# Kernel tuning notes

Hardware: AMD Instinct MI355X
Metric: run time of the kernel (lower is better)

Reference implementation:

```python
import jax, jax.numpy as jnp
import numpy as np

B, LT, LE, D, H, M, BS = 4, 2048, 1024, 1024, 16, 4096, 128
HD = D // H            # head dim 64
NB = LT // BS          # 16 blocks
SINK_ITERS = 5
NEG = -1e9
SCALE = 1.0 / np.sqrt(HD).astype(np.float32)


def setup_inputs() -> dict:
    key = jax.random.key(0)
    ks = jax.random.split(key, 16)
    p = lambda k, shp: jax.random.normal(k, shp, jnp.float32) * 0.02
    return {
        "targets": jax.random.normal(ks[0], (B, LT, D), jnp.float32),
        "encoded": jax.random.normal(ks[1], (B, LE, D), jnp.float32),
        "ln1_s": jnp.ones((D,), jnp.float32), "ln1_b": jnp.zeros((D,), jnp.float32),
        "ln2_s": jnp.ones((D,), jnp.float32), "ln2_b": jnp.zeros((D,), jnp.float32),
        "ln3_s": jnp.ones((D,), jnp.float32), "ln3_b": jnp.zeros((D,), jnp.float32),
        "wq1": p(ks[2], (D, H, HD)), "wk1": p(ks[3], (D, H, HD)),
        "wv1": p(ks[4], (D, H, HD)), "wo1": p(ks[5], (H, HD, D)),
        "wsort": p(ks[6], (H, HD, NB)),
        "wq2": p(ks[7], (D, H, HD)), "wk2": p(ks[8], (D, H, HD)),
        "wv2": p(ks[9], (D, H, HD)), "wo2": p(ks[10], (H, HD, D)),
        "w1": p(ks[11], (D, M)), "b1": jnp.zeros((M,), jnp.float32),
        "w2": p(ks[12], (M, D)), "b2": jnp.zeros((D,), jnp.float32),
    }


def layer_norm(x, s, b, eps=1e-6):
    mu = jnp.mean(x, -1, keepdims=True)
    var = jnp.mean(jnp.square(x - mu), -1, keepdims=True)
    return (x - mu) * jax.lax.rsqrt(var + eps) * s + b


def causal_sinkhorn(logits):
    # logits: [B,H,NB,NB]. Causal block mask + iterative log-space row/col
    # normalization -> soft (doubly-stochastic-ish) block permutation matrix.
    mask = jnp.tril(jnp.ones((NB, NB), bool))
    la = jnp.where(mask, logits, NEG)
    for _ in range(SINK_ITERS):
        la = la - jax.nn.logsumexp(la, axis=-1, keepdims=True)
        la = jnp.where(mask, la, NEG)
        la = la - jax.nn.logsumexp(la, axis=-2, keepdims=True)
        la = jnp.where(mask, la, NEG)
    return jnp.exp(la)


def sinkhorn_self_attention(x, wq, wk, wv, wsort, wo):
    # x: [B,LT,D] -> blocked q/k/v: [B,NB,BS,H,HD]
    q = jnp.einsum('bld,dhk->blhk', x, wq).reshape(B, NB, BS, H, HD)
    k = jnp.einsum('bld,dhk->blhk', x, wk).reshape(B, NB, BS, H, HD)
    v = jnp.einsum('bld,dhk->blhk', x, wv).reshape(B, NB, BS, H, HD)
    # SortNet: sum-pooled block key representations -> block-to-block logits
    krep = jnp.sum(k, axis=2)                                   # [B,NB,H,HD]
    P = causal_sinkhorn(jnp.einsum('bnhk,hkm->bhnm', krep, wsort))  # [B,H,NB,NB]
    ks = jnp.einsum('bhij,bjshk->bishk', P, k)                  # sorted key blocks
    vs = jnp.einsum('bhij,bjshk->bishk', P, v)
    # each query block attends to (own block [causal]) ++ (sorted block)
    s_loc = jnp.einsum('bnqhk,bnshk->bhnqs', q, k) * SCALE      # [B,H,NB,BS,BS]
    s_srt = jnp.einsum('bnqhk,bnshk->bhnqs', q, ks) * SCALE
    cm = jnp.tril(jnp.ones((BS, BS), bool))
    s_loc = jnp.where(cm, s_loc, NEG)
    w = jax.nn.softmax(jnp.concatenate([s_loc, s_srt], axis=-1), axis=-1)
    o = (jnp.einsum('bhnqs,bnshk->bnqhk', w[..., :BS], v)
         + jnp.einsum('bhnqs,bnshk->bnqhk', w[..., BS:], vs))
    return jnp.einsum('blhk,hkd->bld', o.reshape(B, LT, H, HD), wo)


def cross_attention(x, kv, wq, wk, wv, wo):
    q = jnp.einsum('bld,dhk->blhk', x, wq)
    k = jnp.einsum('bld,dhk->blhk', kv, wk)
    v = jnp.einsum('bld,dhk->blhk', kv, wv)
    w = jax.nn.softmax(jnp.einsum('bqhk,bshk->bhqs', q, k) * SCALE, axis=-1)
    o = jnp.einsum('bhqs,bshk->bqhk', w, v)
    return jnp.einsum('blhk,hkd->bld', o, wo)


def reference(targets, encoded, ln1_s, ln1_b, ln2_s, ln2_b, ln3_s, ln3_b,
              wq1, wk1, wv1, wo1, wsort, wq2, wk2, wv2, wo2, w1, b1, w2, b2):
    x = layer_norm(targets, ln1_s, ln1_b)
    x = sinkhorn_self_attention(x, wq1, wk1, wv1, wsort, wo1) + targets
    y = layer_norm(x, ln2_s, ln2_b)
    y = cross_attention(y, encoded, wq2, wk2, wv2, wo2) + x
    z = layer_norm(y, ln3_s, ln3_b)
    z = jnp.dot(jax.nn.gelu(jnp.dot(z, w1) + b1), w2) + b2
    return y + z
```

## Files before the change

### kernel.cpp

```cpp
#include <hip/hip_runtime.h>

typedef unsigned short u16;
typedef __attribute__((ext_vector_type(8))) short short8;
typedef __attribute__((ext_vector_type(4))) short short4_t;
typedef __attribute__((ext_vector_type(4))) float float4_t;

#define B_ 4
#define LT_ 2048
#define LE_ 1024
#define D_ 1024
#define H_ 16
#define HD_ 64
#define NB_ 16
#define BS_ 128
#define M_ 4096
#define SCALE_ 0.125f

typedef __attribute__((address_space(1))) const void gas_t;
typedef __attribute__((address_space(3))) void las_t;

__device__ __forceinline__ float b2f(u16 u) {
  union { unsigned int i; float f; } v; v.i = ((unsigned int)u) << 16; return v.f;
}
__device__ __forceinline__ u16 f2b(float f) {
  union { float f; unsigned int i; } v; v.f = f;
  unsigned int x = v.i;
  return (u16)((x + 0x7fffu + ((x >> 16) & 1u)) >> 16);
}
__device__ __forceinline__ float gelu_f(float u) {
  float t = 0.7978845608028654f * (u + 0.044715f * u * u * u);
  float th = 1.f - 2.f / (__expf(2.f * t) + 1.f);
  return 0.5f * u * (1.f + th);
}
__device__ __forceinline__ void store_val(u16* p, float x) { *p = f2b(x); }
__device__ __forceinline__ void store_val(float* p, float x) { *p = x; }

__global__ __launch_bounds__(256)
void conv_k(const float* __restrict__ in, u16* __restrict__ out) {
  int i = (blockIdx.x * 256 + threadIdx.x) * 4;
  float4_t v = *(const float4_t*)(in + i);
  short4_t o;
  o[0] = (short)f2b(v[0]); o[1] = (short)f2b(v[1]);
  o[2] = (short)f2b(v[2]); o[3] = (short)f2b(v[3]);
  *(short4_t*)(out + i) = o;
}

__global__ __launch_bounds__(256)
void transpose_k(const float* __restrict__ in, u16* __restrict__ out, int R, int rstride) {
  __shared__ u16 tile[32][33];
  int bx = blockIdx.x * 32, by = blockIdx.y * 32;
  int tx = threadIdx.x & 31, ty = threadIdx.x >> 5;
  #pragma unroll
  for (int y = ty; y < 32; y += 8)
    tile[y][tx] = f2b(in[(size_t)(by + y) * rstride + bx + tx]);
  __syncthreads();
  #pragma unroll
  for (int y = ty; y < 32; y += 8)
    out[(size_t)(bx + y) * R + by + tx] = tile[tx][y];
}

#define NJOBS 10
struct TJobs {
  const float* src[NJOBS];
  u16* dst[NJOBS];
  int outR[NJOBS];
  int inS[NJOBS];
  int ntx[NJOBS];
  int ntiles[NJOBS];
};

__global__ __launch_bounds__(256)
void prep_k(TJobs J) {
  int t = blockIdx.x, j = 0;
  while (t >= J.ntiles[j]) { t -= J.ntiles[j]; ++j; }
  const float* in = J.src[j];
  u16* out = J.dst[j];
  const int R = J.outR[j], rstride = J.inS[j];
  const int bx = (t % J.ntx[j]) * 32, by = (t / J.ntx[j]) * 32;
  __shared__ u16 tile[32][33];
  int tx = threadIdx.x & 31, ty = threadIdx.x >> 5;
  #pragma unroll
  for (int y = ty; y < 32; y += 8)
    tile[y][tx] = f2b(in[(size_t)(by + y) * rstride + bx + tx]);
  __syncthreads();
  #pragma unroll
  for (int y = ty; y < 32; y += 8)
    out[(size_t)(bx + y) * R + by + tx] = tile[tx][y];
}

__global__ __launch_bounds__(256)
void ln_k(const float* __restrict__ x, const float* __restrict__ sw,
          const float* __restrict__ bw, u16* __restrict__ out) {
  int row = blockIdx.x, tid = threadIdx.x;
  const float* xr = x + (size_t)row * 1024 + tid * 4;
  float4_t raw = *(const float4_t*)xr;
  float v0 = raw[0], v1 = raw[1], v2 = raw[2], v3 = raw[3];
  float sum = v0 + v1 + v2 + v3;
  #pragma unroll
  for (int off = 32; off > 0; off >>= 1) sum += __shfl_down(sum, off, 64);
  __shared__ float sA[4], sB[4];
  int w = tid >> 6;
  if ((tid & 63) == 0) sA[w] = sum;
  __syncthreads();
  float mu = (sA[0] + sA[1] + sA[2] + sA[3]) * (1.f / 1024.f);
  float d0 = v0 - mu, d1 = v1 - mu, d2 = v2 - mu, d3 = v3 - mu;
  float s2 = d0 * d0 + d1 * d1 + d2 * d2 + d3 * d3;
  #pragma unroll
  for (int off = 32; off > 0; off >>= 1) s2 += __shfl_down(s2, off, 64);
  if ((tid & 63) == 0) sB[w] = s2;
  __syncthreads();
  float inv = rsqrtf((sB[0] + sB[1] + sB[2] + sB[3]) * (1.f / 1024.f) + 1e-6f);
  float4_t sv = *(const float4_t*)(sw + tid * 4);
  float4_t bv = *(const float4_t*)(bw + tid * 4);
  short4_t ov;
  ov[0] = (short)f2b(d0 * inv * sv[0] + bv[0]);
  ov[1] = (short)f2b(d1 * inv * sv[1] + bv[1]);
  ov[2] = (short)f2b(d2 * inv * sv[2] + bv[2]);
  ov[3] = (short)f2b(d3 * inv * sv[3] + bv[3]);
  *(short4_t*)(out + (size_t)row * 1024 + tid * 4) = ov;
}

template<int EPI, typename TC>
__global__ __launch_bounds__(256)
void gemm_k(const u16* __restrict__ A, const u16* __restrict__ Bt,
            const float* __restrict__ bias, const float* __restrict__ res,
            TC* __restrict__ C, int M, int N, int K) {
  __shared__ __align__(16) u16 lA[128 * 32];
  __shared__ __align__(16) u16 lB[128 * 32];
  const int gx = gridDim.x;
  int lin = blockIdx.y * gx + blockIdx.x;
  const int nwg = gx * gridDim.y;
  if (!(nwg & 7)) {
    const int chunk = nwg >> 3;
    lin = (lin & 7) * chunk + (lin >> 3);
  }
  const int bn = (lin % gx) * 128;
  const int bm = (lin / gx) * 128;
  const int tid = threadIdx.x;
  const int lane = tid & 63;
  const int wave = tid >> 6;
  const int wy = wave >> 1, wx = wave & 1;
  const int quad = lane >> 4, l16 = lane & 15;

  float4_t acc[4][4];
  float4_t zz = {0.f, 0.f, 0.f, 0.f};
  #pragma unroll
  for (int i = 0; i < 4; ++i)
    #pragma unroll
    for (int j = 0; j < 4; ++j) acc[i][j] = zz;

  const int r0 = tid >> 2, kc0 = (tid & 3) * 8;
  const u16* gA0 = A + (size_t)(bm + r0) * K + kc0;
  const u16* gA1 = A + (size_t)(bm + 64 + r0) * K + kc0;
  const u16* gB0 = Bt + (size_t)(bn + r0) * K + kc0;
  const u16* gB1 = Bt + (size_t)(bn + 64 + r0) * K + kc0;
  u16* lA0 = &lA[tid * 8];
  u16* lA1 = &lA[(tid + 256) * 8];
  u16* lB0 = &lB[tid * 8];
  u16* lB1 = &lB[(tid + 256) * 8];

  for (int k0 = 0; k0 < K; k0 += 32) {
    __syncthreads();
    __builtin_amdgcn_global_load_lds((gas_t*)(gA0 + k0), (las_t*)lA0, 16, 0, 0);
    __builtin_amdgcn_global_load_lds((gas_t*)(gA1 + k0), (las_t*)lA1, 16, 0, 0);
    __builtin_amdgcn_global_load_lds((gas_t*)(gB0 + k0), (las_t*)lB0, 16, 0, 0);
    __builtin_amdgcn_global_load_lds((gas_t*)(gB1 + k0), (las_t*)lB1, 16, 0, 0);
    __syncthreads();
    short8 af[4], bfr[4];
    #pragma unroll
    for (int i = 0; i < 4; ++i)
      af[i] = *(const short8*)&lA[(wy * 64 + i * 16 + l16) * 32 + quad * 8];
    #pragma unroll
    for (int j = 0; j < 4; ++j)
      bfr[j] = *(const short8*)&lB[(wx * 64 + j * 16 + l16) * 32 + quad * 8];
    #pragma unroll
    for (int i = 0; i < 4; ++i)
      #pragma unroll
      for (int j = 0; j < 4; ++j)
        acc[i][j] = __builtin_amdgcn_mfma_f32_16x16x32_bf16(af[i], bfr[j], acc[i][j], 0, 0, 0);
  }

  #pragma unroll
  for (int i = 0; i < 4; ++i) {
    int row = bm + wy * 64 + i * 16 + quad * 4;
    #pragma unroll
    for (int j = 0; j < 4; ++j) {
      int col = bn + wx * 64 + j * 16 + l16;
      #pragma unroll
      for (int v = 0; v < 4; ++v) {
        float x = acc[i][j][v];
        size_t idx = (size_t)(row + v) * N + col;
        if (EPI == 1) {
          x += res[idx];
        } else if (EPI == 2) {
          x = gelu_f(x + bias[col]);
        } else if (EPI == 3) {
          x += bias[col] + res[idx];
        }
        store_val(&C[idx], x);
      }
    }
  }
}

__global__ __launch_bounds__(256)
void krep_k(const u16* __restrict__ K1, float* __restrict__ krep) {
  int idx = blockIdx.x * 256 + threadIdx.x;
  int col = idx & 1023;
  int bn = idx >> 10;
  const u16* p = K1 + (size_t)bn * 128 * 1024 + col;
  float s = 0.f;
  for (int i = 0; i < 128; ++i) s += b2f(p[(size_t)i * 1024]);
  krep[idx] = s;
}

__global__ __launch_bounds__(256)
void sinkhorn_k(const float* __restrict__ krep, const float* __restrict__ wsort,
                float* __restrict__ P) {
  int bh = blockIdx.x;
  int b = bh >> 4, h = bh & 15;
  int t = threadIdx.x;
  int i = t >> 4, j = t & 15;
  __shared__ float la[16][17];
  __shared__ float red[16];
  float acc = 0.f;
  const float* kr = krep + ((size_t)b * 16 + i) * 1024 + h * 64;
  const float* ws = wsort + (size_t)h * 64 * 16 + j;
  for (int k = 0; k < 64; ++k) acc += kr[k] * ws[k * 16];
  la[i][j] = (j <= i) ? acc : -1e9f;
  __syncthreads();
  for (int it = 0; it < 5; ++it) {
    if (t < 16) {
      float m = -1e30f;
      for (int jj = 0; jj < 16; ++jj) m = fmaxf(m, la[t][jj]);
      float s = 0.f;
      for (int jj = 0; jj < 16; ++jj) s += __expf(la[t][jj] - m);
      red[t] = m + __logf(s);
    }
    __syncthreads();
    la[i][j] = (j <= i) ? la[i][j] - red[i] : -1e9f;
    __syncthreads();
    if (t < 16) {
      float m = -1e30f;
      for (int ii = 0; ii < 16; ++ii) m = fmaxf(m, la[ii][t]);
      float s = 0.f;
      for (int ii = 0; ii < 16; ++ii) s += __expf(la[ii][t] - m);
      red[t] = m + __logf(s);
    }
    __syncthreads();
    la[i][j] = (j <= i) ? la[i][j] - red[j] : -1e9f;
    __syncthreads();
  }
  P[((size_t)bh * 16 + i) * 16 + j] = __expf(la[i][j]);
}

__global__ __launch_bounds__(256)
void sortmix_k(const float* __restrict__ P, const u16* __restrict__ K1,
               const u16* __restrict__ V1, u16* __restrict__ KS,
               u16* __restrict__ VS) {
  int t = blockIdx.x * 256 + threadIdx.x;
  int col = (t & 127) * 8;
  int rest = t >> 7;
  int b = rest >> 11, is = rest & 2047, i = is >> 7, s = is & 127;
  int h = col >> 6;
  const float* Pr = P + (((size_t)(b * 16 + h)) * 16 + i) * 16;
  size_t base = ((size_t)(b * 2048 + s)) * 1024 + col;
  float ka[8] = {0, 0, 0, 0, 0, 0, 0, 0}, va[8] = {0, 0, 0, 0, 0, 0, 0, 0};
  for (int j = 0; j <= i; ++j) {
    float p = Pr[j];
    short8 kk = *(const short8*)&K1[base + (size_t)j * 131072];
    short8 vv = *(const short8*)&V1[base + (size_t)j * 131072];
    #pragma unroll
    for (int e = 0; e < 8; ++e) {
      ka[e] += p * b2f((u16)kk[e]);
      va[e] += p * b2f((u16)vv[e]);
    }
  }
  size_t ob = ((size_t)(b * 2048 + i * 128 + s)) * 1024 + col;
  short8 ok, ov;
  #pragma unroll
  for (int e = 0; e < 8; ++e) { ok[e] = (short)f2b(ka[e]); ov[e] = (short)f2b(va[e]); }
  *(short8*)&KS[ob] = ok;
  *(short8*)&VS[ob] = ov;
}

#define KLS 72
#define VTS 136
#define PLS 136

template<int CROSS>
__global__ __launch_bounds__(256)
void attn_mfma_k(const u16* __restrict__ Q, const u16* __restrict__ Ka,
                 const u16* __restrict__ Va, const u16* __restrict__ Kb2,
                 const u16* __restrict__ Vb2, u16* __restrict__ O) {
  __shared__ __align__(16) u16 kls[128 * KLS];
  __shared__ __align__(16) u16 vtls[64 * VTS];
  __shared__ __align__(16) u16 pls[128 * PLS];
  const int blk = blockIdx.x;
  const int n = blk & 15, h = (blk >> 4) & 15, b = blk >> 8;
  const int tid = threadIdx.x, lane = tid & 63, wv = tid >> 6;
  const int quad = lane >> 4, l16 = lane & 15;
  const int m0 = wv * 32;
  const size_t qrowbase = (size_t)b * 2048 + n * 128;

  short8 qa[2][2];
  #pragma unroll
  for (int qi = 0; qi < 2; ++qi)
    #pragma unroll
    for (int ks = 0; ks < 2; ++ks)
      qa[qi][ks] = *(const short8*)&Q[(qrowbase + m0 + qi * 16 + l16) * 1024 +
                                      h * 64 + ks * 32 + quad * 8];

  float4_t acc_o[2][4];
  float mrow[2], lrow[2];
  #pragma unroll
  for (int mi = 0; mi < 2; ++mi) {
    #pragma unroll
    for (int dn = 0; dn < 4; ++dn) acc_o[mi][dn] = {0.f, 0.f, 0.f, 0.f};
    mrow[mi] = -1e30f; lrow[mi] = 0.f;
  }

  const int NT = CROSS ? 8 : 2;
  for (int t = 0; t < NT; ++t) {
    const u16 *Kg, *Vg;
    bool causal = false;
    if (CROSS) {
      size_t kb = ((size_t)b * 1024 + t * 128) * 1024 + h * 64;
      Kg = Ka + kb; Vg = Va + kb;
    } else if (t == 0) {
      size_t kb = qrowbase * 1024 + h * 64;
      Kg = Ka + kb; Vg = Va + kb; causal = true;
    } else {
      size_t kb = qrowbase * 1024 + h * 64;
      Kg = Kb2 + kb; Vg = Vb2 + kb;
    }
    __syncthreads();
    #pragma unroll
    for (int i = 0; i < 4; ++i) {
      int c = tid + i * 256;
      int row = c >> 3, dd = (c & 7) * 8;
      short8 kv = *(const short8*)&Kg[(size_t)row * 1024 + dd];
      *(short8*)&kls[row * KLS + dd] = kv;
      short8 vv = *(const short8*)&Vg[(size_t)row * 1024 + dd];
      #pragma unroll
      for (int e = 0; e < 8; ++e) vtls[(dd + e) * VTS + row] = (u16)vv[e];
    }
    __syncthreads();

    float4_t s[2][8];
    #pragma unroll
    for (int qi = 0; qi < 2; ++qi)
      #pragma unroll
      for (int nj = 0; nj < 8; ++nj) s[qi][nj] = {0.f, 0.f, 0.f, 0.f};
    #pragma unroll
    for (int nj = 0; nj < 8; ++nj) {
      short8 k0 = *(const short8*)&kls[(nj * 16 + l16) * KLS + quad * 8];
      short8 k1 = *(const short8*)&kls[(nj * 16 + l16) * KLS + 32 + quad * 8];
      #pragma unroll
      for (int qi = 0; qi < 2; ++qi) {
        s[qi][nj] = __builtin_amdgcn_mfma_f32_16x16x32_bf16(k0, qa[qi][0], s[qi][nj], 0, 0, 0);
        s[qi][nj] = __builtin_amdgcn_mfma_f32_16x16x32_bf16(k1, qa[qi][1], s[qi][nj], 0, 0, 0);
      }
    }

    float crv[2];
    #pragma unroll
    for (int qi = 0; qi < 2; ++qi) {
      const int qrow = m0 + qi * 16 + l16;
      float mx = -1e30f;
      #pragma unroll
      for (int nj = 0; nj < 8; ++nj)
        #pragma unroll
        for (int v = 0; v < 4; ++v) {
          float x = s[qi][nj][v] * SCALE_;
          if (causal && (nj * 16 + quad * 4 + v > qrow)) x = -1e30f;
          s[qi][nj][v] = x;
          mx = fmaxf(mx, x);
        }
      mx = fmaxf(mx, __shfl_xor(mx, 16, 64));
      mx = fmaxf(mx, __shfl_xor(mx, 32, 64));
      float mn = fmaxf(mrow[qi], mx);
      crv[qi] = __expf(mrow[qi] - mn);
      mrow[qi] = mn;
      float rs = 0.f;
      #pragma unroll
      for (int nj = 0; nj < 8; ++nj)
        #pragma unroll
        for (int v = 0; v < 4; ++v) {
          float p = __expf(s[qi][nj][v] - mn);
          s[qi][nj][v] = p;
          rs += p;
        }
      rs += __shfl_xor(rs, 16, 64);
      rs += __shfl_xor(rs, 32, 64);
      lrow[qi] = lrow[qi] * crv[qi] + rs;
      #pragma unroll
      for (int nj = 0; nj < 8; ++nj) {
        unsigned p01 = (unsigned)f2b(s[qi][nj][0]) | ((unsigned)f2b(s[qi][nj][1]) << 16);
        unsigned p23 = (unsigned)f2b(s[qi][nj][2]) | ((unsigned)f2b(s[qi][nj][3]) << 16);
        *(unsigned*)&pls[qrow * PLS + nj * 16 + quad * 4] = p01;
        *(unsigned*)&pls[qrow * PLS + nj * 16 + quad * 4 + 2] = p23;
      }
    }
    #pragma unroll
    for (int mi = 0; mi < 2; ++mi)
      #pragma unroll
      for (int v = 0; v < 4; ++v) {
        float c = __shfl(crv[mi], quad * 20 + v, 64);
        #pragma unroll
        for (int dn = 0; dn < 4; ++dn) acc_o[mi][dn][v] *= c;
      }

    #pragma unroll
    for (int ks = 0; ks < 4; ++ks) {
      short8 a0 = *(const short8*)&pls[(m0 + l16) * PLS + ks * 32 + quad * 8];
      short8 a1 = *(const short8*)&pls[(m0 + 16 + l16) * PLS + ks * 32 + quad * 8];
      #pragma unroll
      for (int dn = 0; dn < 4; ++dn) {
        short8 bv = *(const short8*)&vtls[(dn * 16 + l16) * VTS + ks * 32 + quad * 8];
        acc_o[0][dn] = __builtin_amdgcn_mfma_f32_16x16x32_bf16(a0, bv, acc_o[0][dn], 0, 0, 0);
        acc_o[1][dn] = __builtin_amdgcn_mfma_f32_16x16x32_bf16(a1, bv, acc_o[1][dn], 0, 0, 0);
      }
    }
  }
  #pragma unroll
  for (int mi = 0; mi < 2; ++mi) {
    float invl = 1.f / lrow[mi];
    #pragma unroll
    for (int v = 0; v < 4; ++v) {
      float inv = __shfl(invl, quad * 20 + v, 64);
      int rowl = m0 + mi * 16 + quad * 4 + v;
      #pragma unroll
      for (int dn = 0; dn < 4; ++dn)
        O[(qrowbase + rowl) * 1024 + h * 64 + dn * 16 + l16] =
            f2b(acc_o[mi][dn][v] * inv);
    }
  }
}

extern "C" void kernel_launch(void* const* d_in, const int* in_sizes, int n_in,
                              void* d_out, int out_size, void* d_ws, size_t ws_size,
                              hipStream_t stream) {
  const float* targets = (const float*)d_in[0];
  const float* encoded = (const float*)d_in[1];
  const float* ln1s = (const float*)d_in[2];
  const float* ln1b = (const float*)d_in[3];
  const float* ln2s = (const float*)d_in[4];
  const float* ln2b = (const float*)d_in[5];
  const float* ln3s = (const float*)d_in[6];
  const float* ln3b = (const float*)d_in[7];
  const float* wq1 = (const float*)d_in[8];
  const float* wk1 = (const float*)d_in[9];
  const float* wv1 = (const float*)d_in[10];
  const float* wo1 = (const float*)d_in[11];
  const float* wsort = (const float*)d_in[12];
  const float* wq2 = (const float*)d_in[13];
  const float* wk2 = (const float*)d_in[14];
  const float* wv2 = (const float*)d_in[15];
  const float* wo2 = (const float*)d_in[16];
  const float* w1 = (const float*)d_in[17];
  const float* b1 = (const float*)d_in[18];
  const float* w2 = (const float*)d_in[19];
  const float* b2 = (const float*)d_in[20];
  float* out = (float*)d_out;
  (void)in_sizes; (void)n_in; (void)out_size;

  char* ws = (char*)d_ws;
  size_t off = 0;
  auto alloc = [&](size_t n) -> char* {
    char* p = ws + off;
    off += (n + 255) & ~(size_t)255;
    return p;
  };

  const size_t NTD = (size_t)B_ * LT_ * D_;
  const size_t NEED_BIG = (size_t)(8 * 2 + 8 + 8) * 1024 * 1024
                        + (size_t)LE_ * B_ * D_ * 2
                        + NTD * 2 * 7
                        + (1u << 20);

  if (ws_size >= NEED_BIG) {
    u16* wq1t = (u16*)alloc((size_t)1024 * 1024 * 2);
    u16* wk1t = (u16*)alloc((size_t)1024 * 1024 * 2);
    u16* wv1t = (u16*)alloc((size_t)1024 * 1024 * 2);
    u16* wo1t = (u16*)alloc((size_t)1024 * 1024 * 2);
    u16* wq2t = (u16*)alloc((size_t)1024 * 1024 * 2);
    u16* wk2t = (u16*)alloc((size_t)1024 * 1024 * 2);
    u16* wv2t = (u16*)alloc((size_t)1024 * 1024 * 2);
    u16* wo2t = (u16*)alloc((size_t)1024 * 1024 * 2);
    u16* w1t = (u16*)alloc((size_t)4096 * 1024 * 2);
    u16* w2t = (u16*)alloc((size_t)1024 * 4096 * 2);
    u16* Eb  = (u16*)alloc((size_t)B_ * LE_ * D_ * 2);
    u16* XLN = (u16*)alloc(NTD * 2);
    u16* Qb  = (u16*)alloc(NTD * 2);
    u16* Kb  = (u16*)alloc(NTD * 2);
    u16* Vb  = (u16*)alloc(NTD * 2);
    u16* KSb = (u16*)alloc(NTD * 2);
    u16* VSb = (u16*)alloc(NTD * 2);
    u16* Ob  = (u16*)alloc(NTD * 2);
    float* KREP = (float*)alloc((size_t)B_ * NB_ * 1024 * 4);
    float* Pm = (float*)alloc((size_t)B_ * H_ * NB_ * NB_ * 4);
    u16* HML = Qb;

    TJobs J;
    const float* srcs[NJOBS] = {wq1, wk1, wv1, wo1, wq2, wk2, wv2, wo2, w1, w2};
    u16* dsts[NJOBS] = {wq1t, wk1t, wv1t, wo1t, wq2t, wk2t, wv2t, wo2t, w1t, w2t};
    int total = 0;
    for (int j = 0; j < NJOBS; ++j) {
      J.src[j] = srcs[j]; J.dst[j] = dsts[j];
      if (j < 8)      { J.outR[j] = 1024; J.inS[j] = 1024; J.ntx[j] = 32;  J.ntiles[j] = 1024; }
      else if (j == 8){ J.outR[j] = 1024; J.inS[j] = 4096; J.ntx[j] = 128; J.ntiles[j] = 4096; }
      else            { J.outR[j] = 4096; J.inS[j] = 1024; J.ntx[j] = 32;  J.ntiles[j] = 4096; }
      total += J.ntiles[j];
    }
    prep_k<<<total, 256, 0, stream>>>(J);
    conv_k<<<4096, 256, 0, stream>>>(encoded, Eb);

    ln_k<<<8192, 256, 0, stream>>>(targets, ln1s, ln1b, XLN);
    gemm_k<0, u16><<<dim3(8, 64), 256, 0, stream>>>(XLN, wq1t, nullptr, nullptr, Qb, 8192, 1024, 1024);
    gemm_k<0, u16><<<dim3(8, 64), 256, 0, stream>>>(XLN, wk1t, nullptr, nullptr, Kb, 8192, 1024, 1024);
    gemm_k<0, u16><<<dim3(8, 64), 256, 0, stream>>>(XLN, wv1t, nullptr, nullptr, Vb, 8192, 1024, 1024);
    krep_k<<<256, 256, 0, stream>>>(Kb, KREP);
    sinkhorn_k<<<64, 256, 0, stream>>>(KREP, wsort, Pm);
    sortmix_k<<<4096, 256, 0, stream>>>(Pm, Kb, Vb, KSb, VSb);
    attn_mfma_k<0><<<1024, 256, 0, stream>>>(Qb, Kb, Vb, KSb, VSb, Ob);
    gemm_k<1, float><<<dim3(8, 64), 256, 0, stream>>>(Ob, wo1t, nullptr, targets, out, 8192, 1024, 1024);
    ln_k<<<8192, 256, 0, stream>>>(out, ln2s, ln2b, XLN);
    gemm_k<0, u16><<<dim3(8, 64), 256, 0, stream>>>(XLN, wq2t, nullptr, nullptr, Qb, 8192, 1024, 1024);
    gemm_k<0, u16><<<dim3(8, 32), 256, 0, stream>>>(Eb, wk2t, nullptr, nullptr, Kb, 4096, 1024, 1024);
    gemm_k<0, u16><<<dim3(8, 32), 256, 0, stream>>>(Eb, wv2t, nullptr, nullptr, Vb, 4096, 1024, 1024);
    attn_mfma_k<1><<<1024, 256, 0, stream>>>(Qb, Kb, Vb, nullptr, nullptr, Ob);
    gemm_k<1, float><<<dim3(8, 64), 256, 0, stream>>>(Ob, wo2t, nullptr, out, out, 8192, 1024, 1024);
    ln_k<<<8192, 256, 0, stream>>>(out, ln3s, ln3b, XLN);
    gemm_k<2, u16><<<dim3(32, 64), 256, 0, stream>>>(XLN, w1t, b1, nullptr, HML, 8192, 4096, 1024);
    gemm_k<3, float><<<dim3(8, 64), 256, 0, stream>>>(HML, w2t, b2, out, out, 8192, 1024, 4096);
    return;
  }

  const size_t SLC = (size_t)LT_ * D_;
  u16* wT  = (u16*)alloc((size_t)1024 * 1024 * 2);
  u16* XLN = (u16*)alloc(SLC * 2);
  u16* Qb  = (u16*)alloc(SLC * 2);
  u16* Kb  = (u16*)alloc(SLC * 2);
  u16* Vb  = (u16*)alloc(SLC * 2);
  u16* KSb = (u16*)alloc(SLC * 2);
  u16* VSb = (u16*)alloc(SLC * 2);
  u16* Ob  = (u16*)alloc(SLC * 2);
  u16* Hc  = (u16*)alloc(SLC * 2);
  u16* Eb  = (u16*)alloc((size_t)LE_ * D_ * 2);
  float* KREP = (float*)alloc((size_t)NB_ * 1024 * 4);
  float* Pm = (float*)alloc((size_t)H_ * NB_ * NB_ * 4);

  auto T = [&](const float* src, int rs) {
    transpose_k<<<dim3(32, 32), 256, 0, stream>>>(src, wT, 1024, rs);
  };

  for (int b = 0; b < B_; ++b) {
    const float* tgt_b = targets + (size_t)b * SLC;
    const float* enc_b = encoded + (size_t)b * LE_ * D_;
    float* out_b = out + (size_t)b * SLC;

    ln_k<<<2048, 256, 0, stream>>>(tgt_b, ln1s, ln1b, XLN);
    T(wq1, 1024);
    gemm_k<0, u16><<<dim3(8, 16), 256, 0, stream>>>(XLN, wT, nullptr, nullptr, Qb, 2048, 1024, 1024);
    T(wk1, 1024);
    gemm_k<0, u16><<<dim3(8, 16), 256, 0, stream>>>(XLN, wT, nullptr, nullptr, Kb, 2048, 1024, 1024);
    T(wv1, 1024);
    gemm_k<0, u16><<<dim3(8, 16), 256, 0, stream>>>(XLN, wT, nullptr, nullptr, Vb, 2048, 1024, 1024);
    krep_k<<<64, 256, 0, stream>>>(Kb, KREP);
    sinkhorn_k<<<16, 256, 0, stream>>>(KREP, wsort, Pm);
    sortmix_k<<<1024, 256, 0, stream>>>(Pm, Kb, Vb, KSb, VSb);
    attn_mfma_k<0><<<256, 256, 0, stream>>>(Qb, Kb, Vb, KSb, VSb, Ob);
    T(wo1, 1024);
    gemm_k<1, float><<<dim3(8, 16), 256, 0, stream>>>(Ob, wT, nullptr, tgt_b, out_b, 2048, 1024, 1024);
    ln_k<<<2048, 256, 0, stream>>>(out_b, ln2s, ln2b, XLN);
    conv_k<<<1024, 256, 0, stream>>>(enc_b, Eb);
    T(wq2, 1024);
    gemm_k<0, u16><<<dim3(8, 16), 256, 0, stream>>>(XLN, wT, nullptr, nullptr, Qb, 2048, 1024, 1024);
    T(wk2, 1024);
    gemm_k<0, u16><<<dim3(8, 8), 256, 0, stream>>>(Eb, wT, nullptr, nullptr, Kb, 1024, 1024, 1024);
    T(wv2, 1024);
    gemm_k<0, u16><<<dim3(8, 8), 256, 0, stream>>>(Eb, wT, nullptr, nullptr, Vb, 1024, 1024, 1024);
    attn_mfma_k<1><<<256, 256, 0, stream>>>(Qb, Kb, Vb, nullptr, nullptr, Ob);
    T(wo2, 1024);
    gemm_k<1, float><<<dim3(8, 16), 256, 0, stream>>>(Ob, wT, nullptr, out_b, out_b, 2048, 1024, 1024);
    ln_k<<<2048, 256, 0, stream>>>(out_b, ln3s, ln3b, XLN);
    for (int c = 0; c < 4; ++c) {
      T(w1 + (size_t)c * 1024, 4096);
      gemm_k<2, u16><<<dim3(8, 16), 256, 0, stream>>>(XLN, wT, b1 + c * 1024, nullptr, Hc,
                                                      2048, 1024, 1024);
      T(w2 + (size_t)c * 1024 * 1024, 1024);
      if (c < 3)
        gemm_k<1, float><<<dim3(8, 16), 256, 0, stream>>>(Hc, wT, nullptr, out_b, out_b,
                                                          2048, 1024, 1024);
      else
        gemm_k<3, float><<<dim3(8, 16), 256, 0, stream>>>(Hc, wT, b2, out_b, out_b,
                                                          2048, 1024, 1024);
    }
  }
}
```

Before: 824.5 us.

## Fuse QKV projections into split-output GEMMs and add 256x256 pipelined GEMM kernel

Adds a 256x256-tile, 512-thread GEMM kernel with a 4-stage global_load_lds pipeline and swizzled LDS reads. It is used for a fused Q/K/V projection (N=3072) and the FFN up-projection. The cross-attention K/V projections are fused into one launch using a split-output epilogue that writes each 1024-column slice into a separate buffer. The aim is fewer launches, better operand reuse and more latency hiding, at the cost of relying on the Q/K/V and weight buffers being laid out contiguously at a stride of NTD.

After: 794.3 us. 3.7% less time.

```diff
diff --git a/kernel.cpp b/kernel.cpp
--- a/kernel.cpp
+++ b/kernel.cpp
@@ -120,11 +120,11 @@
   *(short4_t*)(out + (size_t)row * 1024 + tid * 4) = ov;
 }
 
-template<int EPI, typename TC>
+template<int EPI, typename TC, int SPLIT>
 __global__ __launch_bounds__(256)
 void gemm_k(const u16* __restrict__ A, const u16* __restrict__ Bt,
             const float* __restrict__ bias, const float* __restrict__ res,
-            TC* __restrict__ C, int M, int N, int K) {
+            TC* __restrict__ C, int M, int N, int K, size_t cstride) {
   __shared__ __align__(16) u16 lA[128 * 32];
   __shared__ __align__(16) u16 lB[128 * 32];
   const int gx = gridDim.x;
@@ -186,10 +186,13 @@
     #pragma unroll
     for (int j = 0; j < 4; ++j) {
       int col = bn + wx * 64 + j * 16 + l16;
+      TC* Cb = SPLIT ? (C + (size_t)(col >> 10) * cstride) : C;
+      int ccol = SPLIT ? (col & 1023) : col;
+      int cn = SPLIT ? 1024 : N;
       #pragma unroll
       for (int v = 0; v < 4; ++v) {
         float x = acc[i][j][v];
-        size_t idx = (size_t)(row + v) * N + col;
+        size_t idx = (size_t)(row + v) * cn + ccol;
         if (EPI == 1) {
           x += res[idx];
         } else if (EPI == 2) {
@@ -197,7 +200,121 @@
         } else if (EPI == 3) {
           x += bias[col] + res[idx];
         }
-        store_val(&C[idx], x);
+        store_val(&Cb[idx], x);
+      }
+    }
+  }
+}
+
+template<int EPI, typename TC, int SPLIT>
+__global__ __launch_bounds__(512, 2)
+void gemm256_k(const u16* __restrict__ A, const u16* __restrict__ Bt,
+               const float* __restrict__ bias, const float* __restrict__ res,
+               TC* __restrict__ C, int M, int N, int K, size_t cstride) {
+  __shared__ __align__(16) u16 lA[4][256 * 32];
+  __shared__ __align__(16) u16 lB[4][256 * 32];
+  const int gx = gridDim.x;
+  int lin = blockIdx.y * gx + blockIdx.x;
+  const int nwg = gx * gridDim.y;
+  if (!(nwg & 7)) {
+    const int chunk = nwg >> 3;
+    lin = (lin & 7) * chunk + (lin >> 3);
+  }
+  const int bn = (lin % gx) * 256;
+  const int bm = (lin / gx) * 256;
+  const int tid = threadIdx.x;
+  const int lane = tid & 63;
+  const int wave = tid >> 6;
+  const int wy = wave >> 2, wx = wave & 3;
+  const int quad = lane >> 4, l16 = lane & 15;
+  const int slo = ((quad ^ ((l16 >> 1) & 3)) << 4);
+
+  int lrow[2], kcs[2];
+  #pragma unroll
+  for (int u = 0; u < 2; ++u) {
+    int p = (tid + u * 512) * 16;
+    int lg = p ^ (((p >> 7) & 3) << 4);
+    lrow[u] = lg >> 6;
+    kcs[u] = (lg & 63) >> 1;
+  }
+  const u16* gA[2]; const u16* gB[2];
+  #pragma unroll
+  for (int u = 0; u < 2; ++u) {
+    gA[u] = A + (size_t)(bm + lrow[u]) * K + kcs[u];
+    gB[u] = Bt + (size_t)(bn + lrow[u]) * K + kcs[u];
+  }
+  const int NT = K >> 5;
+
+  float4_t acc[8][4];
+  float4_t zz = {0.f, 0.f, 0.f, 0.f};
+  #pragma unroll
+  for (int i = 0; i < 8; ++i)
+    #pragma unroll
+    for (int j = 0; j < 4; ++j) acc[i][j] = zz;
+
+  #define STAGE256(TT, BUF)                                                      \
+    {                                                                            \
+      int kk_ = (TT) * 32;                                                       \
+      __builtin_amdgcn_global_load_lds((gas_t*)(gA[0] + kk_),                    \
+          (las_t*)((char*)&lA[BUF][0] + tid * 16), 16, 0, 0);                    \
+      __builtin_amdgcn_global_load_lds((gas_t*)(gA[1] + kk_),                    \
+          (las_t*)((char*)&lA[BUF][0] + (tid + 512) * 16), 16, 0, 0);            \
+      __builtin_amdgcn_global_load_lds((gas_t*)(gB[0] + kk_),                    \
+          (las_t*)((char*)&lB[BUF][0] + tid * 16), 16, 0, 0);                    \
+      __builtin_amdgcn_global_load_lds((gas_t*)(gB[1] + kk_),                    \
+          (las_t*)((char*)&lB[BUF][0] + (tid + 512) * 16), 16, 0, 0);            \
+    }
+
+  STAGE256(0, 0)
+  STAGE256(1, 1)
+  STAGE256(2, 2)
+
+  for (int t = 0; t < NT; ++t) {
+    asm volatile("s_waitcnt vmcnt(8)" ::: "memory");
+    __builtin_amdgcn_s_barrier();
+    __builtin_amdgcn_sched_barrier(0);
+    int ts = t + 3; if (ts > NT - 1) ts = NT - 1;
+    STAGE256(ts, (t + 3) & 3)
+    const char* bufA = (const char*)&lA[t & 3][0];
+    const char* bufB = (const char*)&lB[t & 3][0];
+    short8 af[8], bf[4];
+    #pragma unroll
+    for (int i = 0; i < 8; ++i)
+      af[i] = *(const short8*)(bufA + (wy * 128 + i * 16 + l16) * 64 + slo);
+    #pragma unroll
+    for (int j = 0; j < 4; ++j)
+      bf[j] = *(const short8*)(bufB + (wx * 64 + j * 16 + l16) * 64 + slo);
+    __builtin_amdgcn_s_setprio(1);
+    #pragma unroll
+    for (int i = 0; i < 8; ++i)
+      #pragma unroll
+      for (int j = 0; j < 4; ++j)
+        acc[i][j] = __builtin_amdgcn_mfma_f32_16x16x32_bf16(af[i], bf[j], acc[i][j], 0, 0, 0);
+    __builtin_amdgcn_s_setprio(0);
+  }
+  #undef STAGE256
+
+  #pragma unroll
+  for (int i = 0; i < 8; ++i) {
+    int row = bm + wy * 128 + i * 16 + quad * 4;
+    #pragma unroll
+    for (int j = 0; j < 4; ++j) {
+      int col = bn + wx * 64 + j * 16 + l16;
+      TC* Cb = SPLIT ? (C + (size_t)(col >> 10) * cstride) : C;
+      int ccol = SPLIT ? (col & 1023) : col;
+      int cn = SPLIT ? 1024 : N;
+      #pragma unroll
+      for (int v = 0; v < 4; ++v) {
+        float x = acc[i][j][v];
+        size_t idx = (size_t)(row + v) * cn + ccol;
+        if (EPI == 1) {
+          x += res[idx];
+        } else if (EPI == 2) {
+          x = gelu_f(x + bias[col]);
+        } else if (EPI == 3) {
+          x += bias[col] + res[idx];
+        }
+        store_val(&Cb[idx], x);
       }
     }
   }
@@ -517,23 +634,21 @@
     conv_k<<<4096, 256, 0, stream>>>(encoded, Eb);
 
     ln_k<<<8192, 256, 0, stream>>>(targets, ln1s, ln1b, XLN);
-    gemm_k<0, u16><<<dim3(8, 64), 256, 0, stream>>>(XLN, wq1t, nullptr, nullptr, Qb, 8192, 1024, 1024);
-    gemm_k<0, u16><<<dim3(8, 64), 256, 0, stream>>>(XLN, wk1t, nullptr, nullptr, Kb, 8192, 1024, 1024);
-    gemm_k<0, u16><<<dim3(8, 64), 256, 0, stream>>>(XLN, wv1t, nullptr, nullptr, Vb, 8192, 1024, 1024);
+    gemm256_k<0, u16, 1><<<dim3(12, 32), 512, 0, stream>>>(XLN, wq1t, nullptr, nullptr,
+                                                           Qb, 8192, 3072, 1024, NTD);
     krep_k<<<256, 256, 0, stream>>>(Kb, KREP);
     sinkhorn_k<<<64, 256, 0, stream>>>(KREP, wsort, Pm);
     sortmix_k<<<4096, 256, 0, stream>>>(Pm, Kb, Vb, KSb, VSb);
     attn_mfma_k<0><<<1024, 256, 0, stream>>>(Qb, Kb, Vb, KSb, VSb, Ob);
-    gemm_k<1, float><<<dim3(8, 64), 256, 0, stream>>>(Ob, wo1t, nullptr, targets, out, 8192, 1024, 1024);
+    gemm_k<1, float, 0><<<dim3(8, 64), 256, 0, stream>>>(Ob, wo1t, nullptr, targets, out, 8192, 1024, 1024, 0);
     ln_k<<<8192, 256, 0, stream>>>(out, ln2s, ln2b, XLN);
-    gemm_k<0, u16><<<dim3(8, 64), 256, 0, stream>>>(XLN, wq2t, nullptr, nullptr, Qb, 8192, 1024, 1024);
-    gemm_k<0, u16><<<dim3(8, 32), 256, 0, stream>>>(Eb, wk2t, nullptr, nullptr, Kb, 4096, 1024, 1024);
-    gemm_k<0, u16><<<dim3(8, 32), 256, 0, stream>>>(Eb, wv2t, nullptr, nullptr, Vb, 4096, 1024, 1024);
+    gemm_k<0, u16, 0><<<dim3(8, 64), 256, 0, stream>>>(XLN, wq2t, nullptr, nullptr, Qb, 8192, 1024, 1024, 0);
+    gemm_k<0, u16, 1><<<dim3(16, 32), 256, 0, stream>>>(Eb, wk2t, nullptr, nullptr, Kb, 4096, 2048, 1024, NTD);
     attn_mfma_k<1><<<1024, 256, 0, stream>>>(Qb, Kb, Vb, nullptr, nullptr, Ob);
-    gemm_k<1, float><<<dim3(8, 64), 256, 0, stream>>>(Ob, wo2t, nullptr, out, out, 8192, 1024, 1024);
+    gemm_k<1, float, 0><<<dim3(8, 64), 256, 0, stream>>>(Ob, wo2t, nullptr, out, out, 8192, 1024, 1024, 0);
     ln_k<<<8192, 256, 0, stream>>>(out, ln3s, ln3b, XLN);
-    gemm_k<2, u16><<<dim3(32, 64), 256, 0, stream>>>(XLN, w1t, b1, nullptr, HML, 8192, 4096, 1024);
-    gemm_k<3, float><<<dim3(8, 64), 256, 0, stream>>>(HML, w2t, b2, out, out, 8192, 1024, 4096);
+    gemm256_k<2, u16, 0><<<dim3(16, 32), 512, 0, stream>>>(XLN, w1t, b1, nullptr, HML, 8192, 4096, 1024, 0);
+    gemm_k<3, float, 0><<<dim3(8, 64), 256, 0, stream>>>(HML, w2t, b2, out, out, 8192, 1024, 4096, 0);
     return;
   }
 
@@ -562,40 +677,40 @@
 
     ln_k<<<2048, 256, 0, stream>>>(tgt_b, ln1s, ln1b, XLN);
     T(wq1, 1024);
-    gemm_k<0, u16><<<dim3(8, 16), 256, 0, stream>>>(XLN, wT, nullptr, nullptr, Qb, 2048, 1024, 1024);
+    gemm_k<0, u16, 0><<<dim3(8, 16), 256, 0, stream>>>(XLN, wT, nullptr, nullptr, Qb, 2048, 1024, 1024, 0);
     T(wk1, 1024);
-    gemm_k<0, u16><<<dim3(8, 16), 256, 0, stream>>>(XLN, wT, nullptr, nullptr, Kb, 2048, 1024, 1024);
+    gemm_k<0, u16, 0><<<dim3(8, 16), 256, 0, stream>>>(XLN, wT, nullptr, nullptr, Kb, 2048, 1024, 1024, 0);
     T(wv1, 1024);
-    gemm_k<0, u16><<<dim3(8, 16), 256, 0, stream>>>(XLN, wT, nullptr, nullptr, Vb, 2048, 1024, 1024);
+    gemm_k<0, u16, 0><<<dim3(8, 16), 256, 0, stream>>>(XLN, wT, nullptr, nullptr, Vb, 2048, 1024, 1024, 0);
     krep_k<<<64, 256, 0, stream>>>(Kb, KREP);
     sinkhorn_k<<<16, 256, 0, stream>>>(KREP, wsort, Pm);
     sortmix_k<<<1024, 256, 0, stream>>>(Pm, Kb, Vb, KSb, VSb);
     attn_mfma_k<0><<<256, 256, 0, stream>>>(Qb, Kb, Vb, KSb, VSb, Ob);
     T(wo1, 1024);
-    gemm_k<1, float><<<dim3(8, 16), 256, 0, stream>>>(Ob, wT, nullptr, tgt_b, out_b, 2048, 1024, 1024);
+    gemm_k<1, float, 0><<<dim3(8, 16), 256, 0, stream>>>(Ob, wT, nullptr, tgt_b, out_b, 2048, 1024, 1024, 0);
     ln_k<<<2048, 256, 0, stream>>>(out_b, ln2s, ln2b, XLN);
     conv_k<<<1024, 256, 0, stream>>>(enc_b, Eb);
     T(wq2, 1024);
-    gemm_k<0, u16><<<dim3(8, 16), 256, 0, stream>>>(XLN, wT, nullptr, nullptr, Qb, 2048, 1024, 1024);
+    gemm_k<0, u16, 0><<<dim3(8, 16), 256, 0, stream>>>(XLN, wT, nullptr, nullptr, Qb, 2048, 1024, 1024, 0);
     T(wk2, 1024);
-    gemm_k<0, u16><<<dim3(8, 8), 256, 0, stream>>>(Eb, wT, nullptr, nullptr, Kb, 1024, 1024, 1024);
+    gemm_k<0, u16, 0><<<dim3(8, 8), 256, 0, stream>>>(Eb, wT, nullptr, nullptr, Kb, 1024, 1024, 1024, 0);
     T(wv2, 1024);
-    gemm_k<0, u16><<<dim3(8, 8), 256, 0, stream>>>(Eb, wT, nullptr, nullptr, Vb, 1024, 1024, 1024);
+    gemm_k<0, u16, 0><<<dim3(8, 8), 256, 0, stream>>>(Eb, wT, nullptr, nullptr, Vb, 1024, 1024, 1024, 0);
     attn_mfma_k<1><<<256, 256, 0, stream>>>(Qb, Kb, Vb, nullptr, nullptr, Ob);
     T(wo2, 1024);
-    gemm_k<1, float><<<dim3(8, 16), 256, 0, stream>>>(Ob, wT, nullptr, out_b, out_b, 2048, 1024, 1024);
+    gemm_k<1, float, 0><<<dim3(8, 16), 256, 0, stream>>>(Ob, wT, nullptr, out_b, out_b, 2048, 1024, 1024, 0);
     ln_k<<<2048, 256, 0, stream>>>(out_b, ln3s, ln3b, XLN);
     for (int c = 0; c < 4; ++c) {
       T(w1 + (size_t)c * 1024, 4096);
-      gemm_k<2, u16><<<dim3(8, 16), 256, 0, stream>>>(XLN, wT, b1 + c * 1024, nullptr, Hc,
-                                                      2048, 1024, 1024);
+      gemm_k<2, u16, 0><<<dim3(8, 16), 256, 0, stream>>>(XLN, wT, b1 + c * 1024, nullptr, Hc,
+                                                         2048, 1024, 1024, 0);
       T(w2 + (size_t)c * 1024 * 1024, 1024);
       if (c < 3)
-        gemm_k<1, float><<<dim3(8, 16), 256, 0, stream>>>(Hc, wT, nullptr, out_b, out_b,
-                                                          2048, 1024, 1024);
+        gemm_k<1, float, 0><<<dim3(8, 16), 256, 0, stream>>>(Hc, wT, nullptr, out_b, out_b,
+                                                             2048, 1024, 1024, 0);
       else
-        gemm_k<3, float><<<dim3(8, 16), 256, 0, stream>>>(Hc, wT, b2, out_b, out_b,
-                                                          2048, 1024, 1024);
-    }
-  }
-}
+        gemm_k<3, float, 0><<<dim3(8, 16), 256, 0, stream>>>(Hc, wT, b2, out_b, out_b,
+                                                             2048, 1024, 1024, 0);
+    }
+  }
+}
```
